# Kernel optimization log

Measured on AMD Instinct MI355X. Metric: run time of the kernel, lower is better.

Reference implementation:

```python
import jax, jax.numpy as jnp
import numpy as np
from jax import lax

VOCAB, EMB, HID, T, B, NCLS = 30000, 100, 128, 200, 512, 9
BN_EPS = 1e-3  # keras BatchNormalization default epsilon


def _lstm(x, W, U, b, reverse):
    # Keras LSTM with activation='relu', recurrent_activation='sigmoid'.
    # x: [B,T,E]; W: [E,4H]; U: [H,4H]; b: [4H]. Gate order: i, f, c, o.
    xz = jnp.einsum('bte,eh->bth', x, W) + b  # precompute input projection [B,T,4H]
    H = U.shape[0]
    Bsz = x.shape[0]

    def step(carry, xz_t):
        h, c = carry
        z = xz_t + h @ U
        zi, zf, zg, zo = jnp.split(z, 4, axis=-1)
        i = jax.nn.sigmoid(zi)
        f = jax.nn.sigmoid(zf)
        g = jax.nn.relu(zg)          # activation='relu' on candidate
        o = jax.nn.sigmoid(zo)
        c = f * c + i * g
        h = o * jax.nn.relu(c)       # activation='relu' on cell output
        return (h, c), h

    init = (jnp.zeros((Bsz, H), x.dtype), jnp.zeros((Bsz, H), x.dtype))
    _, hs = lax.scan(step, init, jnp.swapaxes(xz, 0, 1), reverse=reverse)
    return jnp.swapaxes(hs, 0, 1)  # [B,T,H]


def setup_inputs() -> dict:
    key = jax.random.key(0)
    ks = jax.random.split(key, 12)
    s = 0.05
    return {
        'tokens': jax.random.randint(ks[0], (B, T), 0, VOCAB, dtype=jnp.int32),
        'emb': jax.random.normal(ks[1], (VOCAB, EMB), jnp.float32) * s,
        'Wf': jax.random.normal(ks[2], (EMB, 4 * HID), jnp.float32) * s,
        'Uf': jax.random.normal(ks[3], (HID, 4 * HID), jnp.float32) * s,
        'bf': jnp.zeros((4 * HID,), jnp.float32),
        'Wb': jax.random.normal(ks[4], (EMB, 4 * HID), jnp.float32) * s,
        'Ub': jax.random.normal(ks[5], (HID, 4 * HID), jnp.float32) * s,
        'bb': jnp.zeros((4 * HID,), jnp.float32),
        'gamma': jnp.ones((2 * HID,), jnp.float32),
        'beta': jnp.zeros((2 * HID,), jnp.float32),
        'mov_mean': jax.random.normal(ks[6], (2 * HID,), jnp.float32) * 0.01,
        'mov_var': jnp.ones((2 * HID,), jnp.float32),
        'Wd': jax.random.normal(ks[7], (2 * HID, NCLS), jnp.float32) * s,
        'bd': jnp.zeros((NCLS,), jnp.float32),
    }


def reference(tokens, emb, Wf, Uf, bf, Wb, Ub, bb, gamma, beta, mov_mean, mov_var, Wd, bd):
    x = emb[tokens]                                   # [B,T,EMB]
    h_fwd = _lstm(x, Wf, Uf, bf, reverse=False)       # [B,T,HID]
    h_bwd = _lstm(x, Wb, Ub, bb, reverse=True)        # [B,T,HID]
    h = jnp.concatenate([h_fwd, h_bwd], axis=-1)      # [B,T,2H]
    # BatchNormalization (inference mode, moving stats), dropout is identity at inference
    h = (h - mov_mean) * lax.rsqrt(mov_var + BN_EPS) * gamma + beta
    return jax.nn.softmax(h @ Wd + bd, axis=-1)       # [B,T,NCLS]
```

## Files before the change

### kernel.cpp

```cpp
#include <hip/hip_runtime.h>


#define TT 200

typedef short v8s __attribute__((ext_vector_type(8)));
typedef float v4f __attribute__((ext_vector_type(4)));

__device__ __forceinline__ void block_sync_lds() {
    asm volatile("s_waitcnt lgkmcnt(0)\n\ts_barrier" ::: "memory");
}
__device__ __forceinline__ float bf2f(unsigned short u) {
    unsigned x = ((unsigned)u) << 16;
    return __builtin_bit_cast(float, x);
}
__device__ __forceinline__ unsigned short f2bf(float f) {
    unsigned u = __builtin_bit_cast(unsigned, f);
    u += 0x7fffu + ((u >> 16) & 1u);
    return (unsigned short)(u >> 16);
}
__device__ __forceinline__ float clampf(float x, float c) {
    return fminf(fmaxf(x, -c), c);
}
__device__ __forceinline__ float sigmf(float x) {
    float e = __expf(-fabsf(x));
    float s = __builtin_amdgcn_rcpf(1.0f + e);
    return x >= 0.0f ? s : 1.0f - s;
}
__device__ __forceinline__ bool probe_f32(const void* mvar) {
    return *(const unsigned*)mvar == 0x3F800000u;
}
__device__ __forceinline__ float ldf(const void* p, int i, bool f32) {
    return f32 ? ((const float*)p)[i] : bf2f(((const unsigned short*)p)[i]);
}

__global__ __launch_bounds__(256) void k_cast(const void* __restrict__ emb,
                                              const void* __restrict__ mvar,
                                              unsigned short* __restrict__ emb_b) {
    bool f32 = probe_f32(mvar);
    int n = 3000000;
    for (int i = blockIdx.x * 256 + threadIdx.x; i < n; i += gridDim.x * 256)
        emb_b[i] = f32 ? f2bf(((const float*)emb)[i]) : ((const unsigned short*)emb)[i];
}

__global__ __launch_bounds__(512) void k_prep(
    const void* __restrict__ Wf, const void* __restrict__ Uf,
    const void* __restrict__ Wb, const void* __restrict__ Ub,
    const void* __restrict__ gamma, const void* __restrict__ beta,
    const void* __restrict__ mmean, const void* __restrict__ mvar,
    const void* __restrict__ Wd, const void* __restrict__ bd,
    const void* __restrict__ bfv, const void* __restrict__ bbv,
    unsigned short* __restrict__ WU_T, unsigned short* __restrict__ WlT,
    float* __restrict__ bias_c, float* __restrict__ bdp) {
    bool f32 = probe_f32(mvar);
    int bid = blockIdx.x, tid = threadIdx.x;
    if (bid < 128) {
        int e0 = bid * 2048 + tid * 4;
        int dir = e0 >> 17;
        int n = (e0 >> 8) & 511;
        int k0 = e0 & 255;
        const void* W = dir ? Wb : Wf;
        const void* U = dir ? Ub : Uf;
        unsigned short v[4];
#pragma unroll
        for (int i = 0; i < 4; i++) {
            int k = k0 + i;
            float x = (k < 100) ? ldf(W, k * 512 + n, f32)
                    : (k < 128) ? 0.0f
                                : ldf(U, (k - 128) * 512 + n, f32);
            v[i] = f2bf(x);
        }
        uint2 pk;
        pk.x = (unsigned)v[0] | ((unsigned)v[1] << 16);
        pk.y = (unsigned)v[2] | ((unsigned)v[3] << 16);
        *(uint2*)(WU_T + e0) = pk;
    } else if (bid == 128) {
#pragma unroll
        for (int e = 0; e < 8; e++) {
            int f = tid * 8 + e;
            int dir = f >> 11, j = (f >> 7) & 15, k = f & 127;
            int c = dir * 128 + k;
            unsigned short v = 0;
            if (j < 9) {
                float sc = ldf(gamma, c, f32) * rsqrtf(ldf(mvar, c, f32) + 1e-3f);
                v = f2bf(clampf(sc * ldf(Wd, c * 9 + j, f32), 1e4f));
            }
            WlT[f] = v;
        }
    } else {
        bias_c[tid] = ldf(bfv, tid, f32);
        bias_c[512 + tid] = ldf(bbv, tid, f32);
        if (tid < 9) {
            int j = tid;
            float acc = ldf(bd, j, f32);
            for (int c = 0; c < 256; c++) {
                float sc = ldf(gamma, c, f32) * rsqrtf(ldf(mvar, c, f32) + 1e-3f);
                float sh = ldf(beta, c, f32) - ldf(mmean, c, f32) * sc;
                acc += sh * ldf(Wd, c * 9 + j, f32);
            }
            bdp[j] = clampf(acc, 1e4f);
        }
    }
}

__global__ __launch_bounds__(512, 1) void k_lstm(
    const int* __restrict__ tokens, const unsigned short* __restrict__ emb,
    const unsigned short* __restrict__ WU_T, const unsigned short* __restrict__ WlT,
    const float* __restrict__ bias_c, float* __restrict__ part) {
    __shared__ __attribute__((aligned(16))) unsigned short h_lds[8][16][136];
    __shared__ int tok_lds[16 * TT];

    int tid = threadIdx.x;
    int w = tid >> 6, l = tid & 63;
    int quad = l >> 4, mrow = l & 15;
    int dir = blockIdx.x >> 5, rb = blockIdx.x & 31;

    v8s Bfr[4][8];
#pragma unroll
    for (int G = 0; G < 4; G++) {
        int n = G * 128 + w * 16 + mrow;
        const unsigned short* base = WU_T + ((size_t)(dir * 512 + n)) * 256 + quad * 8;
#pragma unroll
        for (int s = 0; s < 8; s++) Bfr[G][s] = *(const v8s*)(base + s * 32);
    }
    v8s Wl[4];
    {
        const unsigned short* base = WlT + dir * 2048 + mrow * 128 + quad * 8;
#pragma unroll
        for (int s = 0; s < 4; s++) Wl[s] = *(const v8s*)(base + s * 32);
    }
    float bias[4];
#pragma unroll
    for (int G = 0; G < 4; G++) bias[G] = bias_c[dir * 512 + G * 128 + w * 16 + mrow];

    for (int i = tid; i < 8 * 16 * 136; i += 512) ((unsigned short*)h_lds)[i] = 0;
    {
        const int* tsrc = tokens + (size_t)rb * 16 * TT;
        for (int i = tid; i < 16 * TT; i += 512) tok_lds[i] = tsrc[i];
    }
    __syncthreads();

    float cst[4] = {0.f, 0.f, 0.f, 0.f};
    float* ppart = part + (size_t)dir * (102400u * 12u);

#define GATHER_X(dst0, dst1, dst2, dst3, step)                                     \
    {                                                                              \
        int tpos = dir ? (TT - 1 - (step)) : (step);                               \
        int tok = tok_lds[mrow * TT + tpos];                                       \
        const unsigned short* er = emb + (size_t)tok * 100 + quad * 8;             \
        union { uint2 u[2]; v8s v; } a0, a1, a2, a3;                               \
        a0.u[0] = *(const uint2*)er;        a0.u[1] = *(const uint2*)(er + 4);     \
        a1.u[0] = *(const uint2*)(er + 32); a1.u[1] = *(const uint2*)(er + 36);    \
        a2.u[0] = *(const uint2*)(er + 64); a2.u[1] = *(const uint2*)(er + 68);    \
        a3.u[0] = make_uint2(0u, 0u); a3.u[1] = make_uint2(0u, 0u);                \
        if (quad == 0) a3.u[0] = *(const uint2*)(emb + (size_t)tok * 100 + 96);    \
        dst0 = a0.v; dst1 = a1.v; dst2 = a2.v; dst3 = a3.v;                        \
    }

#define XPART(acc, x0, x1, x2, x3)                                                     \
    {                                                                                  \
        acc[0] = (v4f){bias[0], bias[0], bias[0], bias[0]};                            \
        acc[1] = (v4f){bias[1], bias[1], bias[1], bias[1]};                            \
        acc[2] = (v4f){bias[2], bias[2], bias[2], bias[2]};                            \
        acc[3] = (v4f){bias[3], bias[3], bias[3], bias[3]};                            \
        acc[0] = __builtin_amdgcn_mfma_f32_16x16x32_bf16(x0, Bfr[0][0], acc[0], 0, 0, 0); \
        acc[1] = __builtin_amdgcn_mfma_f32_16x16x32_bf16(x0, Bfr[1][0], acc[1], 0, 0, 0); \
        acc[2] = __builtin_amdgcn_mfma_f32_16x16x32_bf16(x0, Bfr[2][0], acc[2], 0, 0, 0); \
        acc[3] = __builtin_amdgcn_mfma_f32_16x16x32_bf16(x0, Bfr[3][0], acc[3], 0, 0, 0); \
        acc[0] = __builtin_amdgcn_mfma_f32_16x16x32_bf16(x1, Bfr[0][1], acc[0], 0, 0, 0); \
        acc[1] = __builtin_amdgcn_mfma_f32_16x16x32_bf16(x1, Bfr[1][1], acc[1], 0, 0, 0); \
        acc[2] = __builtin_amdgcn_mfma_f32_16x16x32_bf16(x1, Bfr[2][1], acc[2], 0, 0, 0); \
        acc[3] = __builtin_amdgcn_mfma_f32_16x16x32_bf16(x1, Bfr[3][1], acc[3], 0, 0, 0); \
        acc[0] = __builtin_amdgcn_mfma_f32_16x16x32_bf16(x2, Bfr[0][2], acc[0], 0, 0, 0); \
        acc[1] = __builtin_amdgcn_mfma_f32_16x16x32_bf16(x2, Bfr[1][2], acc[1], 0, 0, 0); \
        acc[2] = __builtin_amdgcn_mfma_f32_16x16x32_bf16(x2, Bfr[2][2], acc[2], 0, 0, 0); \
        acc[3] = __builtin_amdgcn_mfma_f32_16x16x32_bf16(x2, Bfr[3][2], acc[3], 0, 0, 0); \
        acc[0] = __builtin_amdgcn_mfma_f32_16x16x32_bf16(x3, Bfr[0][3], acc[0], 0, 0, 0); \
        acc[1] = __builtin_amdgcn_mfma_f32_16x16x32_bf16(x3, Bfr[1][3], acc[1], 0, 0, 0); \
        acc[2] = __builtin_amdgcn_mfma_f32_16x16x32_bf16(x3, Bfr[2][3], acc[2], 0, 0, 0); \
        acc[3] = __builtin_amdgcn_mfma_f32_16x16x32_bf16(x3, Bfr[3][3], acc[3], 0, 0, 0); \
    }

    v8s xc0, xc1, xc2, xc3, xn0, xn1, xn2, xn3;
    GATHER_X(xc0, xc1, xc2, xc3, 0);
    GATHER_X(xn0, xn1, xn2, xn3, 1);
    v4f accx[4];
    XPART(accx, xc0, xc1, xc2, xc3);

    for (int it = 0; it <= TT; ++it) {
        if ((it & 7) == 0 && it) {
            int s = it - 8 + w;
            v8s hg0 = *(const v8s*)&h_lds[w][mrow][quad * 8];
            v8s hg1 = *(const v8s*)&h_lds[w][mrow][32 + quad * 8];
            v8s hg2 = *(const v8s*)&h_lds[w][mrow][64 + quad * 8];
            v8s hg3 = *(const v8s*)&h_lds[w][mrow][96 + quad * 8];
            v4f la = {0.f, 0.f, 0.f, 0.f};
            la = __builtin_amdgcn_mfma_f32_16x16x32_bf16(hg0, Wl[0], la, 0, 0, 0);
            la = __builtin_amdgcn_mfma_f32_16x16x32_bf16(hg1, Wl[1], la, 0, 0, 0);
            la = __builtin_amdgcn_mfma_f32_16x16x32_bf16(hg2, Wl[2], la, 0, 0, 0);
            la = __builtin_amdgcn_mfma_f32_16x16x32_bf16(hg3, Wl[3], la, 0, 0, 0);
            if (mrow < 9) {
                int tpos = dir ? (TT - 1 - s) : s;
                float* pp = ppart + ((size_t)(rb * 16 + quad * 4) * TT + tpos) * 12 + mrow;
#pragma unroll
                for (int r = 0; r < 4; r++) pp[r * (TT * 12)] = la[r];
            }
            block_sync_lds();
        }
        if (it == TT) break;

        int rs = (it - 1) & 7;
        v8s ha0 = *(const v8s*)&h_lds[rs][mrow][quad * 8];
        v8s ha1 = *(const v8s*)&h_lds[rs][mrow][32 + quad * 8];
        v8s ha2 = *(const v8s*)&h_lds[rs][mrow][64 + quad * 8];
        v8s ha3 = *(const v8s*)&h_lds[rs][mrow][96 + quad * 8];

        v4f acc[4] = {accx[0], accx[1], accx[2], accx[3]};
        acc[0] = __builtin_amdgcn_mfma_f32_16x16x32_bf16(ha0, Bfr[0][4], acc[0], 0, 0, 0);
        acc[1] = __builtin_amdgcn_mfma_f32_16x16x32_bf16(ha0, Bfr[1][4], acc[1], 0, 0, 0);
        acc[2] = __builtin_amdgcn_mfma_f32_16x16x32_bf16(ha0, Bfr[2][4], acc[2], 0, 0, 0);
        acc[3] = __builtin_amdgcn_mfma_f32_16x16x32_bf16(ha0, Bfr[3][4], acc[3], 0, 0, 0);
        acc[0] = __builtin_amdgcn_mfma_f32_16x16x32_bf16(ha1, Bfr[0][5], acc[0], 0, 0, 0);
        acc[1] = __builtin_amdgcn_mfma_f32_16x16x32_bf16(ha1, Bfr[1][5], acc[1], 0, 0, 0);
        acc[2] = __builtin_amdgcn_mfma_f32_16x16x32_bf16(ha1, Bfr[2][5], acc[2], 0, 0, 0);
        acc[3] = __builtin_amdgcn_mfma_f32_16x16x32_bf16(ha1, Bfr[3][5], acc[3], 0, 0, 0);
        acc[0] = __builtin_amdgcn_mfma_f32_16x16x32_bf16(ha2, Bfr[0][6], acc[0], 0, 0, 0);
        acc[1] = __builtin_amdgcn_mfma_f32_16x16x32_bf16(ha2, Bfr[1][6], acc[1], 0, 0, 0);
        acc[2] = __builtin_amdgcn_mfma_f32_16x16x32_bf16(ha2, Bfr[2][6], acc[2], 0, 0, 0);
        acc[3] = __builtin_amdgcn_mfma_f32_16x16x32_bf16(ha2, Bfr[3][6], acc[3], 0, 0, 0);
        acc[0] = __builtin_amdgcn_mfma_f32_16x16x32_bf16(ha3, Bfr[0][7], acc[0], 0, 0, 0);
        acc[1] = __builtin_amdgcn_mfma_f32_16x16x32_bf16(ha3, Bfr[1][7], acc[1], 0, 0, 0);
        acc[2] = __builtin_amdgcn_mfma_f32_16x16x32_bf16(ha3, Bfr[2][7], acc[2], 0, 0, 0);
        acc[3] = __builtin_amdgcn_mfma_f32_16x16x32_bf16(ha3, Bfr[3][7], acc[3], 0, 0, 0);

        v8s xf0, xf1, xf2, xf3;
        bool pf = (it + 2 < TT);
        if (pf) GATHER_X(xf0, xf1, xf2, xf3, it + 2);

        v4f accx2[4];
        if (it + 1 < TT) {
            XPART(accx2, xn0, xn1, xn2, xn3);
        }

        unsigned short hbits[4];
#pragma unroll
        for (int r = 0; r < 4; r++) {
            float i_ = sigmf(acc[0][r]);
            float f_ = sigmf(acc[1][r]);
            float g_ = fmaxf(acc[2][r], 0.0f);
            float o_ = sigmf(acc[3][r]);
            float c_ = f_ * cst[r] + i_ * g_;
            cst[r] = c_;
            hbits[r] = f2bf(o_ * fmaxf(c_, 0.0f));
        }
        int wsl = it & 7;
#pragma unroll
        for (int r = 0; r < 4; r++) h_lds[wsl][quad * 4 + r][w * 16 + mrow] = hbits[r];
        block_sync_lds();

#pragma unroll
        for (int G = 0; G < 4; G++) accx[G] = accx2[G];
        xc0 = xn0; xc1 = xn1; xc2 = xn2; xc3 = xn3;
        if (pf) { xn0 = xf0; xn1 = xf1; xn2 = xf2; xn3 = xf3; }
    }
#undef GATHER_X
#undef XPART
}

__global__ __launch_bounds__(256) void k_head(const float* __restrict__ part,
                                              const float* __restrict__ bdp,
                                              float* __restrict__ out) {
    int tid = threadIdx.x;
    int tok0 = blockIdx.x * 256 + tid;
    float bias[9];
#pragma unroll
    for (int j = 0; j < 9; j++) bias[j] = bdp[j];
#pragma unroll
    for (int u = 0; u < 2; u++) {
        int tok = tok0 + u * 51200;
        const float* p0 = part + (size_t)tok * 12;
        const float* p1 = part + (size_t)(102400 + tok) * 12;
        v4f a0 = *(const v4f*)p0, a1 = *(const v4f*)(p0 + 4);
        float a8 = p0[8];
        v4f b0 = *(const v4f*)p1, b1 = *(const v4f*)(p1 + 4);
        float b8 = p1[8];
        float lg[9];
#pragma unroll
        for (int j = 0; j < 4; j++) lg[j] = clampf(a0[j] + b0[j] + bias[j], 1e4f);
#pragma unroll
        for (int j = 0; j < 4; j++) lg[4 + j] = clampf(a1[j] + b1[j] + bias[4 + j], 1e4f);
        lg[8] = clampf(a8 + b8 + bias[8], 1e4f);
        float m = lg[0];
#pragma unroll
        for (int j = 1; j < 9; j++) m = fmaxf(m, lg[j]);
        float e[9], s = 0.f;
#pragma unroll
        for (int j = 0; j < 9; j++) { e[j] = __expf(lg[j] - m); s += e[j]; }
        float r = 1.0f / s;
        size_t base = (size_t)tok * 9;
#pragma unroll
        for (int j = 0; j < 9; j++) out[base + j] = e[j] * r;
    }
}

extern "C" void kernel_launch(void* const* d_in, const int* in_sizes, int n_in,
                              void* d_out, int out_size, void* d_ws, size_t ws_size,
                              hipStream_t stream) {
    const int* tokens = (const int*)d_in[0];
    const void* emb = d_in[1];
    const void* Wf = d_in[2];
    const void* Uf = d_in[3];
    const void* bfv = d_in[4];
    const void* Wb = d_in[5];
    const void* Ub = d_in[6];
    const void* bbv = d_in[7];
    const void* gamma = d_in[8];
    const void* beta = d_in[9];
    const void* mmean = d_in[10];
    const void* mvar = d_in[11];
    const void* Wd = d_in[12];
    const void* bd = d_in[13];

    char* ws = (char*)d_ws;
    unsigned short* WU_T = (unsigned short*)ws;
    unsigned short* WlT = (unsigned short*)(ws + 524288);
    float* bias_c = (float*)(ws + 532480);
    float* bdp = (float*)(ws + 536576);
    unsigned short* emb_b = (unsigned short*)(ws + 536640);
    float* part = (float*)(ws + 6536640);

    k_cast<<<1024, 256, 0, stream>>>(emb, mvar, emb_b);
    k_prep<<<130, 512, 0, stream>>>(Wf, Uf, Wb, Ub, gamma, beta, mmean, mvar, Wd, bd,
                                    bfv, bbv, WU_T, WlT, bias_c, bdp);
    k_lstm<<<64, 512, 0, stream>>>(tokens, emb_b, WU_T, WlT, bias_c, part);
    k_head<<<200, 256, 0, stream>>>(part, bdp, (float*)d_out);
}
```

Measured before the change: 423.9 us.

## Halve LSTM block to 4 waves with 32 hidden units each, unroll steps

The recurrent kernel now runs 256 threads per block, with each wave owning 32 hidden columns (8 MFMA N-tiles) instead of 16. This halves the number of waves taking part in each per-step barrier and gives each wave more independent MFMAs to interleave. The time loop is unrolled by two with ping-pong accumulators, and the h history ring grows to 16 slots so logits are computed every 8 steps by 4 waves over two groups. Logit weights move to LDS, and the sigmoid becomes a single exp plus reciprocal. In exchange the register footprint doubles (64 B-fragments per lane), which risks spills, and each wave's serial chain per step gets longer.

```diff
diff --git a/kernel.cpp b/kernel.cpp
--- a/kernel.cpp
+++ b/kernel.cpp
@@ -22,9 +22,7 @@
     return fminf(fmaxf(x, -c), c);
 }
 __device__ __forceinline__ float sigmf(float x) {
-    float e = __expf(-fabsf(x));
-    float s = __builtin_amdgcn_rcpf(1.0f + e);
-    return x >= 0.0f ? s : 1.0f - s;
+    return __builtin_amdgcn_rcpf(1.0f + __expf(-x));
 }
 __device__ __forceinline__ bool probe_f32(const void* mvar) {
     return *(const unsigned*)mvar == 0x3F800000u;
@@ -102,50 +100,50 @@
     }
 }
 
-__global__ __launch_bounds__(512, 1) void k_lstm(
+__global__ __launch_bounds__(256, 1) void k_lstm(
     const int* __restrict__ tokens, const unsigned short* __restrict__ emb,
     const unsigned short* __restrict__ WU_T, const unsigned short* __restrict__ WlT,
     const float* __restrict__ bias_c, float* __restrict__ part) {
-    __shared__ __attribute__((aligned(16))) unsigned short h_lds[8][16][136];
+    __shared__ __attribute__((aligned(16))) unsigned short h_lds[16][16][136];
+    __shared__ __attribute__((aligned(16))) unsigned short wl_lds[2048];
     __shared__ int tok_lds[16 * TT];
 
     int tid = threadIdx.x;
     int w = tid >> 6, l = tid & 63;
     int quad = l >> 4, mrow = l & 15;
     int dir = blockIdx.x >> 5, rb = blockIdx.x & 31;
-
-    v8s Bfr[4][8];
-#pragma unroll
-    for (int G = 0; G < 4; G++) {
-        int n = G * 128 + w * 16 + mrow;
+    int tbase = mrow * TT;
+
+    v8s Bfr[8][8];
+#pragma unroll
+    for (int q = 0; q < 8; q++) {
+        int n = (q >> 1) * 128 + w * 32 + (q & 1) * 16 + mrow;
         const unsigned short* base = WU_T + ((size_t)(dir * 512 + n)) * 256 + quad * 8;
 #pragma unroll
-        for (int s = 0; s < 8; s++) Bfr[G][s] = *(const v8s*)(base + s * 32);
-    }
-    v8s Wl[4];
-    {
-        const unsigned short* base = WlT + dir * 2048 + mrow * 128 + quad * 8;
-#pragma unroll
-        for (int s = 0; s < 4; s++) Wl[s] = *(const v8s*)(base + s * 32);
-    }
-    float bias[4];
-#pragma unroll
-    for (int G = 0; G < 4; G++) bias[G] = bias_c[dir * 512 + G * 128 + w * 16 + mrow];
-
-    for (int i = tid; i < 8 * 16 * 136; i += 512) ((unsigned short*)h_lds)[i] = 0;
+        for (int s = 0; s < 8; s++) Bfr[q][s] = *(const v8s*)(base + s * 32);
+    }
+    v4f bacc[8];
+#pragma unroll
+    for (int q = 0; q < 8; q++) {
+        float b = bias_c[dir * 512 + (q >> 1) * 128 + w * 32 + (q & 1) * 16 + mrow];
+        bacc[q] = (v4f){b, b, b, b};
+    }
+
+    for (int i = tid; i < 16 * 16 * 136; i += 256) ((unsigned short*)h_lds)[i] = 0;
+    for (int i = tid; i < 2048; i += 256) wl_lds[i] = WlT[dir * 2048 + i];
     {
         const int* tsrc = tokens + (size_t)rb * 16 * TT;
-        for (int i = tid; i < 16 * TT; i += 512) tok_lds[i] = tsrc[i];
+        for (int i = tid; i < 16 * TT; i += 256) tok_lds[i] = tsrc[i];
     }
     __syncthreads();
 
-    float cst[4] = {0.f, 0.f, 0.f, 0.f};
+    float cst[8] = {0.f, 0.f, 0.f, 0.f, 0.f, 0.f, 0.f, 0.f};
     float* ppart = part + (size_t)dir * (102400u * 12u);
 
-#define GATHER_X(dst0, dst1, dst2, dst3, step)                                     \
+#define GATHER_X(d0, d1, d2, d3, step)                                             \
     {                                                                              \
         int tpos = dir ? (TT - 1 - (step)) : (step);                               \
-        int tok = tok_lds[mrow * TT + tpos];                                       \
+        int tok = tok_lds[tbase + tpos];                                           \
         const unsigned short* er = emb + (size_t)tok * 100 + quad * 8;             \
         union { uint2 u[2]; v8s v; } a0, a1, a2, a3;                               \
         a0.u[0] = *(const uint2*)er;        a0.u[1] = *(const uint2*)(er + 4);     \
@@ -153,117 +151,103 @@
         a2.u[0] = *(const uint2*)(er + 64); a2.u[1] = *(const uint2*)(er + 68);    \
         a3.u[0] = make_uint2(0u, 0u); a3.u[1] = make_uint2(0u, 0u);                \
         if (quad == 0) a3.u[0] = *(const uint2*)(emb + (size_t)tok * 100 + 96);    \
-        dst0 = a0.v; dst1 = a1.v; dst2 = a2.v; dst3 = a3.v;                        \
-    }
-
-#define XPART(acc, x0, x1, x2, x3)                                                     \
-    {                                                                                  \
-        acc[0] = (v4f){bias[0], bias[0], bias[0], bias[0]};                            \
-        acc[1] = (v4f){bias[1], bias[1], bias[1], bias[1]};                            \
-        acc[2] = (v4f){bias[2], bias[2], bias[2], bias[2]};                            \
-        acc[3] = (v4f){bias[3], bias[3], bias[3], bias[3]};                            \
-        acc[0] = __builtin_amdgcn_mfma_f32_16x16x32_bf16(x0, Bfr[0][0], acc[0], 0, 0, 0); \
-        acc[1] = __builtin_amdgcn_mfma_f32_16x16x32_bf16(x0, Bfr[1][0], acc[1], 0, 0, 0); \
-        acc[2] = __builtin_amdgcn_mfma_f32_16x16x32_bf16(x0, Bfr[2][0], acc[2], 0, 0, 0); \
-        acc[3] = __builtin_amdgcn_mfma_f32_16x16x32_bf16(x0, Bfr[3][0], acc[3], 0, 0, 0); \
-        acc[0] = __builtin_amdgcn_mfma_f32_16x16x32_bf16(x1, Bfr[0][1], acc[0], 0, 0, 0); \
-        acc[1] = __builtin_amdgcn_mfma_f32_16x16x32_bf16(x1, Bfr[1][1], acc[1], 0, 0, 0); \
-        acc[2] = __builtin_amdgcn_mfma_f32_16x16x32_bf16(x1, Bfr[2][1], acc[2], 0, 0, 0); \
-        acc[3] = __builtin_amdgcn_mfma_f32_16x16x32_bf16(x1, Bfr[3][1], acc[3], 0, 0, 0); \
-        acc[0] = __builtin_amdgcn_mfma_f32_16x16x32_bf16(x2, Bfr[0][2], acc[0], 0, 0, 0); \
-        acc[1] = __builtin_amdgcn_mfma_f32_16x16x32_bf16(x2, Bfr[1][2], acc[1], 0, 0, 0); \
-        acc[2] = __builtin_amdgcn_mfma_f32_16x16x32_bf16(x2, Bfr[2][2], acc[2], 0, 0, 0); \
-        acc[3] = __builtin_amdgcn_mfma_f32_16x16x32_bf16(x2, Bfr[3][2], acc[3], 0, 0, 0); \
-        acc[0] = __builtin_amdgcn_mfma_f32_16x16x32_bf16(x3, Bfr[0][3], acc[0], 0, 0, 0); \
-        acc[1] = __builtin_amdgcn_mfma_f32_16x16x32_bf16(x3, Bfr[1][3], acc[1], 0, 0, 0); \
-        acc[2] = __builtin_amdgcn_mfma_f32_16x16x32_bf16(x3, Bfr[2][3], acc[2], 0, 0, 0); \
-        acc[3] = __builtin_amdgcn_mfma_f32_16x16x32_bf16(x3, Bfr[3][3], acc[3], 0, 0, 0); \
-    }
-
-    v8s xc0, xc1, xc2, xc3, xn0, xn1, xn2, xn3;
-    GATHER_X(xc0, xc1, xc2, xc3, 0);
-    GATHER_X(xn0, xn1, xn2, xn3, 1);
-    v4f accx[4];
-    XPART(accx, xc0, xc1, xc2, xc3);
-
-    for (int it = 0; it <= TT; ++it) {
-        if ((it & 7) == 0 && it) {
-            int s = it - 8 + w;
-            v8s hg0 = *(const v8s*)&h_lds[w][mrow][quad * 8];
-            v8s hg1 = *(const v8s*)&h_lds[w][mrow][32 + quad * 8];
-            v8s hg2 = *(const v8s*)&h_lds[w][mrow][64 + quad * 8];
-            v8s hg3 = *(const v8s*)&h_lds[w][mrow][96 + quad * 8];
-            v4f la = {0.f, 0.f, 0.f, 0.f};
-            la = __builtin_amdgcn_mfma_f32_16x16x32_bf16(hg0, Wl[0], la, 0, 0, 0);
-            la = __builtin_amdgcn_mfma_f32_16x16x32_bf16(hg1, Wl[1], la, 0, 0, 0);
-            la = __builtin_amdgcn_mfma_f32_16x16x32_bf16(hg2, Wl[2], la, 0, 0, 0);
-            la = __builtin_amdgcn_mfma_f32_16x16x32_bf16(hg3, Wl[3], la, 0, 0, 0);
-            if (mrow < 9) {
-                int tpos = dir ? (TT - 1 - s) : s;
-                float* pp = ppart + ((size_t)(rb * 16 + quad * 4) * TT + tpos) * 12 + mrow;
-#pragma unroll
-                for (int r = 0; r < 4; r++) pp[r * (TT * 12)] = la[r];
-            }
-            block_sync_lds();
-        }
-        if (it == TT) break;
-
-        int rs = (it - 1) & 7;
-        v8s ha0 = *(const v8s*)&h_lds[rs][mrow][quad * 8];
-        v8s ha1 = *(const v8s*)&h_lds[rs][mrow][32 + quad * 8];
-        v8s ha2 = *(const v8s*)&h_lds[rs][mrow][64 + quad * 8];
-        v8s ha3 = *(const v8s*)&h_lds[rs][mrow][96 + quad * 8];
-
-        v4f acc[4] = {accx[0], accx[1], accx[2], accx[3]};
-        acc[0] = __builtin_amdgcn_mfma_f32_16x16x32_bf16(ha0, Bfr[0][4], acc[0], 0, 0, 0);
-        acc[1] = __builtin_amdgcn_mfma_f32_16x16x32_bf16(ha0, Bfr[1][4], acc[1], 0, 0, 0);
-        acc[2] = __builtin_amdgcn_mfma_f32_16x16x32_bf16(ha0, Bfr[2][4], acc[2], 0, 0, 0);
-        acc[3] = __builtin_amdgcn_mfma_f32_16x16x32_bf16(ha0, Bfr[3][4], acc[3], 0, 0, 0);
-        acc[0] = __builtin_amdgcn_mfma_f32_16x16x32_bf16(ha1, Bfr[0][5], acc[0], 0, 0, 0);
-        acc[1] = __builtin_amdgcn_mfma_f32_16x16x32_bf16(ha1, Bfr[1][5], acc[1], 0, 0, 0);
-        acc[2] = __builtin_amdgcn_mfma_f32_16x16x32_bf16(ha1, Bfr[2][5], acc[2], 0, 0, 0);
-        acc[3] = __builtin_amdgcn_mfma_f32_16x16x32_bf16(ha1, Bfr[3][5], acc[3], 0, 0, 0);
-        acc[0] = __builtin_amdgcn_mfma_f32_16x16x32_bf16(ha2, Bfr[0][6], acc[0], 0, 0, 0);
-        acc[1] = __builtin_amdgcn_mfma_f32_16x16x32_bf16(ha2, Bfr[1][6], acc[1], 0, 0, 0);
-        acc[2] = __builtin_amdgcn_mfma_f32_16x16x32_bf16(ha2, Bfr[2][6], acc[2], 0, 0, 0);
-        acc[3] = __builtin_amdgcn_mfma_f32_16x16x32_bf16(ha2, Bfr[3][6], acc[3], 0, 0, 0);
-        acc[0] = __builtin_amdgcn_mfma_f32_16x16x32_bf16(ha3, Bfr[0][7], acc[0], 0, 0, 0);
-        acc[1] = __builtin_amdgcn_mfma_f32_16x16x32_bf16(ha3, Bfr[1][7], acc[1], 0, 0, 0);
-        acc[2] = __builtin_amdgcn_mfma_f32_16x16x32_bf16(ha3, Bfr[2][7], acc[2], 0, 0, 0);
-        acc[3] = __builtin_amdgcn_mfma_f32_16x16x32_bf16(ha3, Bfr[3][7], acc[3], 0, 0, 0);
-
-        v8s xf0, xf1, xf2, xf3;
-        bool pf = (it + 2 < TT);
-        if (pf) GATHER_X(xf0, xf1, xf2, xf3, it + 2);
-
-        v4f accx2[4];
-        if (it + 1 < TT) {
-            XPART(accx2, xn0, xn1, xn2, xn3);
-        }
-
-        unsigned short hbits[4];
-#pragma unroll
-        for (int r = 0; r < 4; r++) {
-            float i_ = sigmf(acc[0][r]);
-            float f_ = sigmf(acc[1][r]);
-            float g_ = fmaxf(acc[2][r], 0.0f);
-            float o_ = sigmf(acc[3][r]);
-            float c_ = f_ * cst[r] + i_ * g_;
-            cst[r] = c_;
-            hbits[r] = f2bf(o_ * fmaxf(c_, 0.0f));
-        }
-        int wsl = it & 7;
-#pragma unroll
-        for (int r = 0; r < 4; r++) h_lds[wsl][quad * 4 + r][w * 16 + mrow] = hbits[r];
-        block_sync_lds();
-
-#pragma unroll
-        for (int G = 0; G < 4; G++) accx[G] = accx2[G];
-        xc0 = xn0; xc1 = xn1; xc2 = xn2; xc3 = xn3;
-        if (pf) { xn0 = xf0; xn1 = xf1; xn2 = xf2; xn3 = xf3; }
-    }
+        d0 = a0.v; d1 = a1.v; d2 = a2.v; d3 = a3.v;                                \
+    }
+
+#define XPART(AN, X0, X1, X2, X3)                                                  \
+    {                                                                              \
+        _Pragma("unroll") for (int q = 0; q < 8; q++)                              \
+            AN[q] = __builtin_amdgcn_mfma_f32_16x16x32_bf16(X0, Bfr[q][0], bacc[q], 0, 0, 0); \
+        _Pragma("unroll") for (int q = 0; q < 8; q++)                              \
+            AN[q] = __builtin_amdgcn_mfma_f32_16x16x32_bf16(X1, Bfr[q][1], AN[q], 0, 0, 0);   \
+        _Pragma("unroll") for (int q = 0; q < 8; q++)                              \
+            AN[q] = __builtin_amdgcn_mfma_f32_16x16x32_bf16(X2, Bfr[q][2], AN[q], 0, 0, 0);   \
+        _Pragma("unroll") for (int q = 0; q < 8; q++)                              \
+            AN[q] = __builtin_amdgcn_mfma_f32_16x16x32_bf16(X3, Bfr[q][3], AN[q], 0, 0, 0);   \
+    }
+
+#define HPART(AC, h0, h1, h2, h3)                                                  \
+    {                                                                              \
+        _Pragma("unroll") for (int q = 0; q < 8; q++)                              \
+            AC[q] = __builtin_amdgcn_mfma_f32_16x16x32_bf16(h0, Bfr[q][4], AC[q], 0, 0, 0); \
+        _Pragma("unroll") for (int q = 0; q < 8; q++)                              \
+            AC[q] = __builtin_amdgcn_mfma_f32_16x16x32_bf16(h1, Bfr[q][5], AC[q], 0, 0, 0); \
+        _Pragma("unroll") for (int q = 0; q < 8; q++)                              \
+            AC[q] = __builtin_amdgcn_mfma_f32_16x16x32_bf16(h2, Bfr[q][6], AC[q], 0, 0, 0); \
+        _Pragma("unroll") for (int q = 0; q < 8; q++)                              \
+            AC[q] = __builtin_amdgcn_mfma_f32_16x16x32_bf16(h3, Bfr[q][7], AC[q], 0, 0, 0); \
+    }
+
+#define LOGITS(ITV)                                                                \
+    {                                                                              \
+        const unsigned short* wbase = wl_lds + mrow * 128 + quad * 8;              \
+        v8s wl0 = *(const v8s*)(wbase);                                            \
+        v8s wl1 = *(const v8s*)(wbase + 32);                                       \
+        v8s wl2 = *(const v8s*)(wbase + 64);                                       \
+        v8s wl3 = *(const v8s*)(wbase + 96);                                       \
+        _Pragma("unroll") for (int g = 0; g < 2; g++) {                            \
+            int s = (ITV)-8 + w + 4 * g;                                           \
+            int sl = s & 15;                                                       \
+            v8s hg0 = *(const v8s*)&h_lds[sl][mrow][quad * 8];                     \
+            v8s hg1 = *(const v8s*)&h_lds[sl][mrow][32 + quad * 8];                \
+            v8s hg2 = *(const v8s*)&h_lds[sl][mrow][64 + quad * 8];                \
+            v8s hg3 = *(const v8s*)&h_lds[sl][mrow][96 + quad * 8];                \
+            v4f la = {0.f, 0.f, 0.f, 0.f};                                         \
+            la = __builtin_amdgcn_mfma_f32_16x16x32_bf16(hg0, wl0, la, 0, 0, 0);   \
+            la = __builtin_amdgcn_mfma_f32_16x16x32_bf16(hg1, wl1, la, 0, 0, 0);   \
+            la = __builtin_amdgcn_mfma_f32_16x16x32_bf16(hg2, wl2, la, 0, 0, 0);   \
+            la = __builtin_amdgcn_mfma_f32_16x16x32_bf16(hg3, wl3, la, 0, 0, 0);   \
+            if (mrow < 9) {                                                        \
+                int tpos = dir ? (TT - 1 - s) : s;                                 \
+                float* pp = ppart + ((size_t)(rb * 16 + quad * 4) * TT + tpos) * 12 + mrow; \
+                _Pragma("unroll") for (int r = 0; r < 4; r++) pp[r * (TT * 12)] = la[r];    \
+            }                                                                      \
+        }                                                                          \
+    }
+
+#define STEP(ITV, AC, AN, XC0, XC1, XC2, XC3, XN0, XN1, XN2, XN3, DOLOG)           \
+    {                                                                              \
+        if ((ITV) + 2 < TT) GATHER_X(XN0, XN1, XN2, XN3, (ITV) + 2);               \
+        if (DOLOG && (ITV) && (((ITV) & 7) == 0)) LOGITS(ITV);                     \
+        int rs = ((ITV)-1) & 15;                                                   \
+        v8s ha0 = *(const v8s*)&h_lds[rs][mrow][quad * 8];                         \
+        v8s ha1 = *(const v8s*)&h_lds[rs][mrow][32 + quad * 8];                    \
+        v8s ha2 = *(const v8s*)&h_lds[rs][mrow][64 + quad * 8];                    \
+        v8s ha3 = *(const v8s*)&h_lds[rs][mrow][96 + quad * 8];                    \
+        if ((ITV) + 1 < TT) XPART(AN, XC0, XC1, XC2, XC3);                         \
+        HPART(AC, ha0, ha1, ha2, ha3);                                             \
+        int ws = (ITV) & 15;                                                       \
+        _Pragma("unroll") for (int nt = 0; nt < 2; nt++) {                         \
+            _Pragma("unroll") for (int r = 0; r < 4; r++) {                        \
+                float i_ = sigmf(AC[nt][r]);                                       \
+                float f_ = sigmf(AC[2 + nt][r]);                                   \
+                float g_ = fmaxf(AC[4 + nt][r], 0.0f);                             \
+                float o_ = sigmf(AC[6 + nt][r]);                                   \
+                float c_ = f_ * cst[nt * 4 + r] + i_ * g_;                         \
+                cst[nt * 4 + r] = c_;                                              \
+                h_lds[ws][quad * 4 + r][w * 32 + nt * 16 + mrow] =                 \
+                    f2bf(o_ * fmaxf(c_, 0.0f));                                    \
+            }                                                                      \
+        }                                                                          \
+        block_sync_lds();                                                          \
+    }
+
+    v8s xA0, xA1, xA2, xA3, xB0, xB1, xB2, xB3;
+    v4f accA[8], accB[8];
+    GATHER_X(xA0, xA1, xA2, xA3, 0);
+    XPART(accA, xA0, xA1, xA2, xA3);
+    GATHER_X(xB0, xB1, xB2, xB3, 1);
+
+    for (int it = 0; it < TT; it += 2) {
+        STEP(it, accA, accB, xB0, xB1, xB2, xB3, xA0, xA1, xA2, xA3, 1);
+        STEP(it + 1, accB, accA, xA0, xA1, xA2, xA3, xB0, xB1, xB2, xB3, 0);
+    }
+    LOGITS(TT);
 #undef GATHER_X
 #undef XPART
+#undef HPART
+#undef LOGITS
+#undef STEP
 }
 
 __global__ __launch_bounds__(256) void k_head(const float* __restrict__ part,
@@ -331,6 +315,6 @@
     k_cast<<<1024, 256, 0, stream>>>(emb, mvar, emb_b);
     k_prep<<<130, 512, 0, stream>>>(Wf, Uf, Wb, Ub, gamma, beta, mmean, mvar, Wd, bd,
                                     bfv, bbv, WU_T, WlT, bias_c, bdp);
-    k_lstm<<<64, 512, 0, stream>>>(tokens, emb_b, WU_T, WlT, bias_c, part);
+    k_lstm<<<64, 256, 0, stream>>>(tokens, emb_b, WU_T, WlT, bias_c, part);
     k_head<<<200, 256, 0, stream>>>(part, bdp, (float*)d_out);
 }
```

After: 451.7 us. 6.6% more time.
